# Optimization experiments

Hardware: AMD Instinct MI355X
Metric: run time of the kernel (lower is better)

The kernel has to match this reference:

```python
import jax, jax.numpy as jnp
import numpy as np

B, SQ, SKV, E, H = 4, 2048, 2048, 1024, 16
HD = E // H  # 64


def stablemax(x):
    # StableMax: s(x) = x+1 if x>=0 else 1/(1-x), normalized along last axis
    s = jnp.where(x >= 0, x + 1.0, 1.0 / (1.0 - x))
    return s / jnp.sum(s, axis=-1, keepdims=True)


def setup_inputs() -> dict:
    key = jax.random.key(0)
    ks = jax.random.split(key, 6)
    scale = 1.0 / np.sqrt(E)
    return {
        "query": jax.random.normal(ks[0], (B, SQ, E), jnp.float32),
        "key_value": jax.random.normal(ks[1], (B, SKV, E), jnp.float32),
        "Wq": jax.random.normal(ks[2], (E, E), jnp.float32) * scale,
        "bq": jnp.zeros((E,), jnp.float32),
        "Wk": jax.random.normal(ks[3], (E, E), jnp.float32) * scale,
        "bk": jnp.zeros((E,), jnp.float32),
        "Wv": jax.random.normal(ks[4], (E, E), jnp.float32) * scale,
        "bv": jnp.zeros((E,), jnp.float32),
        "Wo": jax.random.normal(ks[5], (E, E), jnp.float32) * scale,
        "bo": jnp.zeros((E,), jnp.float32),
    }


def reference(query, key_value, Wq, bq, Wk, bk, Wv, bv, Wo, bo):
    b = query.shape[0]
    # linear projections (torch Linear: x @ W^T + b)
    q = query @ Wq.T + bq
    k = key_value @ Wk.T + bk
    v = key_value @ Wv.T + bv
    # [B, H, S, HD]
    q = q.reshape(b, -1, H, HD).transpose(0, 2, 1, 3)
    k = k.reshape(b, -1, H, HD).transpose(0, 2, 1, 3)
    v = v.reshape(b, -1, H, HD).transpose(0, 2, 1, 3)
    scores = jnp.einsum("bhqd,bhkd->bhqk", q, k) / np.sqrt(HD).astype(np.float32)
    attn = stablemax(scores)  # dropout is identity in eval mode
    context = jnp.einsum("bhqk,bhkd->bhqd", attn, v)
    context = context.transpose(0, 2, 1, 3).reshape(b, -1, E)
    return context @ Wo.T + bo
```

## Files before the change

kernel.cpp:

```cpp
#include <hip/hip_runtime.h>

typedef __bf16 bf16;
typedef __bf16 bf16x8 __attribute__((ext_vector_type(8)));
typedef __bf16 bf16x4 __attribute__((ext_vector_type(4)));
typedef _Float16 f16;
typedef _Float16 f16x2 __attribute__((ext_vector_type(2)));
typedef _Float16 f16x4 __attribute__((ext_vector_type(4)));
typedef _Float16 f16x8 __attribute__((ext_vector_type(8)));
typedef __fp16 h16x2 __attribute__((ext_vector_type(2)));
typedef float f32x4 __attribute__((ext_vector_type(4)));

__device__ __forceinline__ f32x4 mfma_qk(bf16x8 a, bf16x8 b, f32x4 c) {
    return __builtin_amdgcn_mfma_f32_16x16x32_bf16(a, b, c, 0, 0, 0);
}
__device__ __forceinline__ f32x4 mfma_pv32(f16x8 a, f16x8 b, f32x4 c) {
    return __builtin_amdgcn_mfma_f32_16x16x32_f16(a, b, c, 0, 0, 0);
}
__device__ __forceinline__ f16x2 pkrtz(float a, float b) {
    h16x2 r = __builtin_amdgcn_cvt_pkrtz(a, b);
    return __builtin_bit_cast(f16x2, r);
}

#define GLOAD_LDS16(gp, lp)                                                    \
    __builtin_amdgcn_global_load_lds(                                          \
        (const __attribute__((address_space(1))) unsigned int*)(gp),           \
        (__attribute__((address_space(3))) unsigned int*)(lp), 16, 0, 0)

__global__ __launch_bounds__(256) void cast_inputs(
    const float* __restrict__ w0, const float* __restrict__ w1,
    const float* __restrict__ w2, const float* __restrict__ w3,
    const float* __restrict__ kv, const float* __restrict__ q,
    bf16* __restrict__ Wb, bf16* __restrict__ KVa, bf16* __restrict__ Qb) {
    long i4 = (long)blockIdx.x * 256 + threadIdx.x;
    const float* src;
    bf16* dst;
    long loc;
    float sc = 1.0f;
    if (i4 < 1048576) {
        int which = (int)(i4 >> 18);
        loc = (i4 & 262143) << 2;
        src = which == 0 ? w0 : which == 1 ? w1 : which == 2 ? w2 : w3;
        dst = Wb + ((long)which << 20);
        if (which == 0) sc = 0.125f;
    } else if (i4 < 3145728) {
        loc = (i4 - 1048576) << 2;
        src = kv; dst = KVa;
    } else {
        loc = (i4 - 3145728) << 2;
        src = q; dst = Qb;
    }
    float4 f = *(const float4*)(src + loc);
    bf16x4 o;
    o[0] = (bf16)(f.x * sc); o[1] = (bf16)(f.y * sc);
    o[2] = (bf16)(f.z * sc); o[3] = (bf16)(f.w * sc);
    *(bf16x4*)(dst + loc) = o;
}

__device__ __forceinline__ void gemm_core(
    const bf16* __restrict__ A, const bf16* __restrict__ Wt,
    const float* __restrict__ bias, void* __restrict__ Yv,
    const int om, bf16* smem, const int n0, const int m0, const float bsc) {
    constexpr int Kd = 1024, Nd = 1024;
    constexpr int TP = 132;
    bf16* As = smem;
    bf16* Bs = smem + 8192;
    const int tid = threadIdx.x;
    const int wid = tid >> 6, lane = tid & 63;
    const int l16 = lane & 15, quad = lane >> 4;
    const int mh = (wid >> 1) * 64, nh = (wid & 1) * 64;

    f32x4 acc[4][4];
#pragma unroll
    for (int i = 0; i < 4; ++i)
#pragma unroll
        for (int j = 0; j < 4; ++j) acc[i][j] = (f32x4){0.f, 0.f, 0.f, 0.f};

    for (int k0 = 0; k0 < Kd; k0 += 64) {
#pragma unroll
        for (int j = 0; j < 4; ++j) {
            const int s = j * 256 + tid;
            const int r = s >> 3, c8 = (s & 7) ^ (r & 7);
            GLOAD_LDS16(A + (long)(m0 + r) * Kd + k0 + c8 * 8, &As[s * 8]);
            GLOAD_LDS16(Wt + (long)(n0 + r) * Kd + k0 + c8 * 8, &Bs[s * 8]);
        }
        __syncthreads();
#pragma unroll
        for (int kc = 0; kc < 2; ++kc) {
            bf16x8 af[4], bq[4];
#pragma unroll
            for (int i = 0; i < 4; ++i) {
                const int row = mh + i * 16 + l16;
                af[i] = *(const bf16x8*)&As[(row * 8 + ((kc * 4 + quad) ^ (row & 7))) * 8];
            }
#pragma unroll
            for (int i = 0; i < 4; ++i) {
                const int row = nh + i * 16 + l16;
                bq[i] = *(const bf16x8*)&Bs[(row * 8 + ((kc * 4 + quad) ^ (row & 7))) * 8];
            }
#pragma unroll
            for (int i = 0; i < 4; ++i)
#pragma unroll
                for (int j = 0; j < 4; ++j)
                    acc[i][j] = mfma_qk(af[i], bq[j], acc[i][j]);
        }
        __syncthreads();
    }

    if (om == 2) {
#pragma unroll
        for (int j = 0; j < 4; ++j) {
            const int col = nh + j * 16 + l16;
            const float bv = bias[n0 + col] * bsc;
#pragma unroll
            for (int i = 0; i < 4; ++i)
#pragma unroll
                for (int p = 0; p < 2; ++p) {
                    f16x2 pk2;
                    pk2[0] = (f16)(acc[i][j][p * 2 + 0] + bv);
                    pk2[1] = (f16)(acc[i][j][p * 2 + 1] + bv);
                    *(f16x2*)&smem[col * TP + mh + i * 16 + quad * 4 + p * 2] = pk2;
                }
        }
        __syncthreads();
        const int b_ = m0 >> 11, skv0 = m0 & 2047;
        const int rowc = tid & 15;
        const int B32 = (rowc >> 2) * 32, g4 = (rowc & 3) * 4;
        const f16* sm = (const f16*)smem;
#pragma unroll
        for (int c = 0; c < 8; ++c) {
            const int col = (tid >> 4) + c * 16;
            const int colg = n0 + col;
            f16x4 lo = *(const f16x4*)&sm[col * TP + B32 + g4];
            f16x4 hi = *(const f16x4*)&sm[col * TP + B32 + 16 + g4];
            f16x8 v = __builtin_shufflevector(lo, hi, 0, 1, 2, 3, 4, 5, 6, 7);
            const long base = ((long)((b_ * 16 + (colg >> 6)) * 64 + (colg & 63))) << 11;
            *(f16x8*)((f16*)Yv + base + skv0 + rowc * 8) = v;
        }
    } else {
#pragma unroll
        for (int j = 0; j < 4; ++j) {
            const int col = n0 + nh + j * 16 + l16;
            const float bv = bias[col] * bsc;
#pragma unroll
            for (int i = 0; i < 4; ++i)
#pragma unroll
                for (int r = 0; r < 4; ++r) {
                    int row = m0 + mh + i * 16 + quad * 4 + r;
                    float v = acc[i][j][r] + bv;
                    if (om == 1)
                        ((float*)Yv)[(long)row * Nd + col] = v;
                    else
                        ((bf16*)Yv)[(long)row * Nd + col] = (bf16)v;
                }
        }
    }
}

__global__ __launch_bounds__(256) void proj_qkv(
    const bf16* __restrict__ Qb, const bf16* __restrict__ KVa,
    const bf16* __restrict__ Wb,
    const float* __restrict__ bq, const float* __restrict__ bk,
    const float* __restrict__ bv,
    bf16* __restrict__ Qw, bf16* __restrict__ Kw, f16* __restrict__ Vt) {
    __shared__ __align__(16) bf16 smem[16896];
    const int lin = blockIdx.x + (blockIdx.y << 3) + (blockIdx.z << 9);
    const int nid = (lin & 7) * 192 + (lin >> 3);
    const int z = nid >> 9, rem = nid & 511;
    const int n0 = (rem & 7) << 7, m0 = (rem >> 3) << 7;
    if (z == 0)
        gemm_core(Qb, Wb, bq, Qw, 0, smem, n0, m0, 0.125f);
    else if (z == 1)
        gemm_core(KVa, Wb + (1l << 20), bk, Kw, 0, smem, n0, m0, 1.0f);
    else
        gemm_core(KVa, Wb + (2l << 20), bv, Vt, 2, smem, n0, m0, 1.0f);
}

__global__ __launch_bounds__(256) void gemm_o(
    const bf16* __restrict__ Cw, const bf16* __restrict__ Wo,
    const float* __restrict__ bo, float* __restrict__ out) {
    __shared__ __align__(16) bf16 smem[16896];
    const int lin = blockIdx.x + (blockIdx.y << 3);
    const int nid = (lin & 7) * 64 + (lin >> 3);
    gemm_core(Cw, Wo, bo, out, 1, smem, (nid & 7) << 7, (nid >> 3) << 7, 1.0f);
}

#define PWAIT2 asm volatile("s_waitcnt vmcnt(2) lgkmcnt(0)\ns_barrier" ::: "memory")
#define PWAIT0 asm volatile("s_waitcnt vmcnt(0) lgkmcnt(0)\ns_barrier" ::: "memory")

__global__ __launch_bounds__(256) void attn_kernel(
    const bf16* __restrict__ Q, const bf16* __restrict__ K,
    const f16* __restrict__ Vt, bf16* __restrict__ C) {
    constexpr int E = 1024, S = 2048;
    __shared__ __align__(16) char smem_raw[24576];

    const int tid = threadIdx.x;
    const int wid = tid >> 6, lane = tid & 63;
    const int l16 = lane & 15, quad = lane >> 4;
    const int l7 = l16 & 7, l3 = l16 & 3;
    const int lin = blockIdx.x + (blockIdx.y << 4) + (blockIdx.z << 8);
    const int nid = (lin & 7) * 128 + (lin >> 3);
    const int qt = nid & 15, h = (nid >> 4) & 15, b = nid >> 8;

    const long q0 = (long)b * S + qt * 128;
    const bf16* Qg = Q + q0 * E + h * 64;
    const bf16* Kg = K + (long)b * S * E + h * 64;
    const f16* Vg = Vt + ((long)(b * 16 + h) << 17);

    bf16x8 qf[2][2];
#pragma unroll
    for (int mt = 0; mt < 2; ++mt)
#pragma unroll
        for (int kc = 0; kc < 2; ++kc)
            qf[mt][kc] = *(const bf16x8*)(Qg + (long)(wid * 32 + mt * 16 + l16) * E + kc * 32 + quad * 8);
    asm volatile("s_waitcnt vmcnt(0)" ::: "memory");

    const bf16* Ksrc = Kg + (long)(tid >> 3) * E + (((tid & 7) ^ ((tid >> 3) & 7)) * 8);
    const f16* Vsrc = Vg + (long)(tid >> 2) * S + (((tid & 3) ^ ((tid >> 2) & 3)) * 8);

    int ka0[3], ka1[3], va[3];
#pragma unroll
    for (int i = 0; i < 3; ++i) {
        ka0[i] = i * 8192 + l16 * 128 + ((quad ^ l7) << 4);
        ka1[i] = i * 8192 + l16 * 128 + (((quad + 4) ^ l7) << 4);
        va[i]  = i * 8192 + 4096 + l16 * 64 + ((quad ^ l3) << 4);
    }

    f16x8 ones8;
#pragma unroll
    for (int j = 0; j < 8; ++j) ones8[j] = (f16)1.0f;

    f32x4 ctx[2][4];
    f32x4 dacc[2];
#pragma unroll
    for (int mt = 0; mt < 2; ++mt) {
        dacc[mt] = (f32x4){0.f, 0.f, 0.f, 0.f};
#pragma unroll
        for (int dt = 0; dt < 4; ++dt) ctx[mt][dt] = (f32x4){0.f, 0.f, 0.f, 0.f};
    }

    auto stage = [&](int kv0, int bi) {
        GLOAD_LDS16(Ksrc + (long)kv0 * E, smem_raw + bi * 8192 + tid * 16);
        GLOAD_LDS16(Vsrc + kv0, smem_raw + bi * 8192 + 4096 + tid * 16);
    };

    auto compute = [&](int bi) {
        f32x4 sacc[2][2];
#pragma unroll
        for (int sh = 0; sh < 2; ++sh) {
            bf16x8 kf0 = *(const bf16x8*)(smem_raw + ka0[bi] + sh * 2048);
            bf16x8 kf1 = *(const bf16x8*)(smem_raw + ka1[bi] + sh * 2048);
            __builtin_amdgcn_s_setprio(1);
#pragma unroll
            for (int mt = 0; mt < 2; ++mt) {
                f32x4 t = mfma_qk(kf0, qf[mt][0], (f32x4){0.f, 0.f, 0.f, 0.f});
                sacc[sh][mt] = mfma_qk(kf1, qf[mt][1], t);
            }
            __builtin_amdgcn_s_setprio(0);
        }
        f16x8 pp[2];
#pragma unroll
        for (int mt = 0; mt < 2; ++mt) {
            float sv[8];
#pragma unroll
            for (int sh = 0; sh < 2; ++sh)
#pragma unroll
                for (int r = 0; r < 4; ++r) {
                    float x = sacc[sh][mt][r];
                    float u = __builtin_fabsf(x) + 1.0f;
                    sv[sh * 4 + r] = (x >= 0.f) ? u : __builtin_amdgcn_rcpf(u);
                }
            f16x2 w0 = pkrtz(sv[0], sv[1]);
            f16x2 w1 = pkrtz(sv[2], sv[3]);
            f16x2 w2 = pkrtz(sv[4], sv[5]);
            f16x2 w3 = pkrtz(sv[6], sv[7]);
            f16x4 lo = __builtin_shufflevector(w0, w1, 0, 1, 2, 3);
            f16x4 hi = __builtin_shufflevector(w2, w3, 0, 1, 2, 3);
            pp[mt] = __builtin_shufflevector(lo, hi, 0, 1, 2, 3, 4, 5, 6, 7);
        }
        __builtin_amdgcn_s_setprio(1);
        dacc[0] = mfma_pv32(ones8, pp[0], dacc[0]);
        dacc[1] = mfma_pv32(ones8, pp[1], dacc[1]);
        __builtin_amdgcn_s_setprio(0);
#pragma unroll
        for (int dt = 0; dt < 4; ++dt) {
            f16x8 vf = *(const f16x8*)(smem_raw + va[bi] + dt * 1024);
            __builtin_amdgcn_s_setprio(1);
#pragma unroll
            for (int mt = 0; mt < 2; ++mt)
                ctx[mt][dt] = mfma_pv32(vf, pp[mt], ctx[mt][dt]);
            __builtin_amdgcn_s_setprio(0);
        }
    };

    stage(0, 0);
    stage(32, 1);
    int kv = 64;
#pragma unroll 1
    for (int it = 0; it < 20; ++it) {
        PWAIT2; stage(kv, 2); compute(0); kv += 32;
        PWAIT2; stage(kv, 0); compute(1); kv += 32;
        PWAIT2; stage(kv, 1); compute(2); kv += 32;
    }
    PWAIT2; stage(kv, 2); compute(0);
    PWAIT2; stage(kv + 32, 0); compute(1);
    PWAIT2; compute(2);
    PWAIT0; compute(0);
    __syncthreads();

    float scl[2];
#pragma unroll
    for (int mt = 0; mt < 2; ++mt) scl[mt] = __builtin_amdgcn_rcpf(dacc[mt][0]);

    bf16* Os = (bf16*)smem_raw;
#pragma unroll
    for (int mt = 0; mt < 2; ++mt)
#pragma unroll
        for (int dt = 0; dt < 4; ++dt) {
            bf16x4 o;
#pragma unroll
            for (int r = 0; r < 4; ++r) o[r] = (bf16)(ctx[mt][dt][r] * scl[mt]);
            *(bf16x4*)&Os[(wid * 32 + mt * 16 + l16) * 68 + dt * 16 + quad * 4] = o;
        }
    __syncthreads();
    {
        const int r = tid >> 1, c = (tid & 1) * 32;
        bf16* cp = C + (q0 + r) * E + h * 64 + c;
#pragma unroll
        for (int j = 0; j < 4; ++j)
            *(bf16x8*)(cp + j * 8) = *(const bf16x8*)&Os[r * 68 + c + j * 8];
    }
}

extern "C" void kernel_launch(void* const* d_in, const int* in_sizes, int n_in,
                              void* d_out, int out_size, void* d_ws, size_t ws_size,
                              hipStream_t stream) {
    const float* query = (const float*)d_in[0];
    const float* keyv  = (const float*)d_in[1];
    const float* Wq = (const float*)d_in[2];
    const float* bq = (const float*)d_in[3];
    const float* Wk = (const float*)d_in[4];
    const float* bk = (const float*)d_in[5];
    const float* Wv = (const float*)d_in[6];
    const float* bv = (const float*)d_in[7];
    const float* Wo = (const float*)d_in[8];
    const float* bo = (const float*)d_in[9];

    char* ws = (char*)d_ws;
    bf16* Wb  = (bf16*)ws;
    bf16* KVa = (bf16*)(ws + (8l << 20));
    bf16* Qb  = (bf16*)(ws + (24l << 20));
    bf16* Qw  = (bf16*)(ws + (40l << 20));
    f16*  Vt  = (f16*)(ws + (56l << 20));
    bf16* Kw  = (bf16*)d_out;
    bf16* Cw  = KVa;

    cast_inputs<<<20480, 256, 0, stream>>>(Wq, Wk, Wv, Wo, keyv, query, Wb, KVa, Qb);

    proj_qkv<<<dim3(8, 64, 3), 256, 0, stream>>>(Qb, KVa, Wb, bq, bk, bv, Qw, Kw, Vt);

    attn_kernel<<<dim3(16, 16, 4), 256, 0, stream>>>(Qw, Kw, Vt, Cw);

    gemm_o<<<dim3(8, 64), 256, 0, stream>>>(Cw, Wb + (3l << 20), bo, (float*)d_out);
}
```

Measured before the change: 312.9 us.

## Double KV tile to 64 per stage and compute stablemax reciprocals branch-free with shared rcp

The attention loop now stages 64 KV rows per pipeline stage instead of 32, which halves the number of barrier and wait points. The triple-buffered LDS grows from 24KB to 48KB, and the V layout changes to a 128-byte row swizzle that matches K. The stablemax transform replaces one rcp per element with one rcp per four elements, using products of (|x|+1), and picks between x+1 and the reciprocal with fmax instead of a select. The larger LDS footprint may lower occupancy, and the shared reciprocal adds multiplies and a small extra rounding error.

```diff
diff --git a/kernel.cpp b/kernel.cpp
--- a/kernel.cpp
+++ b/kernel.cpp
@@ -184,19 +184,19 @@
     gemm_core(Cw, Wo, bo, out, 1, smem, (nid & 7) << 7, (nid >> 3) << 7, 1.0f);
 }
 
-#define PWAIT2 asm volatile("s_waitcnt vmcnt(2) lgkmcnt(0)\ns_barrier" ::: "memory")
+#define PWAIT4 asm volatile("s_waitcnt vmcnt(4) lgkmcnt(0)\ns_barrier" ::: "memory")
 #define PWAIT0 asm volatile("s_waitcnt vmcnt(0) lgkmcnt(0)\ns_barrier" ::: "memory")
 
 __global__ __launch_bounds__(256) void attn_kernel(
     const bf16* __restrict__ Q, const bf16* __restrict__ K,
     const f16* __restrict__ Vt, bf16* __restrict__ C) {
     constexpr int E = 1024, S = 2048;
-    __shared__ __align__(16) char smem_raw[24576];
+    __shared__ __align__(16) char smem_raw[49152];
 
     const int tid = threadIdx.x;
     const int wid = tid >> 6, lane = tid & 63;
     const int l16 = lane & 15, quad = lane >> 4;
-    const int l7 = l16 & 7, l3 = l16 & 3;
+    const int l7 = l16 & 7;
     const int lin = blockIdx.x + (blockIdx.y << 4) + (blockIdx.z << 8);
     const int nid = (lin & 7) * 128 + (lin >> 3);
     const int qt = nid & 15, h = (nid >> 4) & 15, b = nid >> 8;
@@ -215,14 +215,15 @@
     asm volatile("s_waitcnt vmcnt(0)" ::: "memory");
 
     const bf16* Ksrc = Kg + (long)(tid >> 3) * E + (((tid & 7) ^ ((tid >> 3) & 7)) * 8);
-    const f16* Vsrc = Vg + (long)(tid >> 2) * S + (((tid & 3) ^ ((tid >> 2) & 3)) * 8);
-
-    int ka0[3], ka1[3], va[3];
+    const f16* Vsrc = Vg + (long)(tid >> 3) * S + (((tid & 7) ^ ((tid >> 3) & 7)) * 8);
+
+    int ka0[3], ka1[3], vaA[3], vaB[3];
 #pragma unroll
     for (int i = 0; i < 3; ++i) {
-        ka0[i] = i * 8192 + l16 * 128 + ((quad ^ l7) << 4);
-        ka1[i] = i * 8192 + l16 * 128 + (((quad + 4) ^ l7) << 4);
-        va[i]  = i * 8192 + 4096 + l16 * 64 + ((quad ^ l3) << 4);
+        ka0[i] = i * 16384 + l16 * 128 + ((quad ^ l7) << 4);
+        ka1[i] = i * 16384 + l16 * 128 + (((quad + 4) ^ l7) << 4);
+        vaA[i] = i * 16384 + 8192 + l16 * 128 + ((quad ^ l7) << 4);
+        vaB[i] = i * 16384 + 8192 + l16 * 128 + (((quad ^ l7) ^ 4) << 4);
     }
 
     f16x8 ones8;
@@ -238,73 +239,93 @@
         for (int dt = 0; dt < 4; ++dt) ctx[mt][dt] = (f32x4){0.f, 0.f, 0.f, 0.f};
     }
 
-    auto stage = [&](int kv0, int bi) {
-        GLOAD_LDS16(Ksrc + (long)kv0 * E, smem_raw + bi * 8192 + tid * 16);
-        GLOAD_LDS16(Vsrc + kv0, smem_raw + bi * 8192 + 4096 + tid * 16);
+    auto stage64 = [&](int kv0, int bi) {
+        char* base = smem_raw + bi * 16384;
+        GLOAD_LDS16(Ksrc + (long)kv0 * E, base + tid * 16);
+        GLOAD_LDS16(Ksrc + (long)(kv0 + 32) * E, base + 4096 + tid * 16);
+        GLOAD_LDS16(Vsrc + kv0, base + 8192 + tid * 16);
+        GLOAD_LDS16(Vsrc + 32 * S + kv0, base + 12288 + tid * 16);
     };
 
-    auto compute = [&](int bi) {
-        f32x4 sacc[2][2];
-#pragma unroll
-        for (int sh = 0; sh < 2; ++sh) {
-            bf16x8 kf0 = *(const bf16x8*)(smem_raw + ka0[bi] + sh * 2048);
-            bf16x8 kf1 = *(const bf16x8*)(smem_raw + ka1[bi] + sh * 2048);
+    auto compute64 = [&](int bi) {
+#pragma unroll
+        for (int kvp = 0; kvp < 2; ++kvp) {
+            bf16x8 kf0[2], kf1[2];
+#pragma unroll
+            for (int sh = 0; sh < 2; ++sh) {
+                const int ko = (kvp * 2 + sh) * 2048;
+                kf0[sh] = *(const bf16x8*)(smem_raw + ka0[bi] + ko);
+                kf1[sh] = *(const bf16x8*)(smem_raw + ka1[bi] + ko);
+            }
+            f32x4 sacc[2][2];
             __builtin_amdgcn_s_setprio(1);
 #pragma unroll
+            for (int sh = 0; sh < 2; ++sh)
+#pragma unroll
+                for (int mt = 0; mt < 2; ++mt) {
+                    f32x4 t = mfma_qk(kf0[sh], qf[mt][0], (f32x4){0.f, 0.f, 0.f, 0.f});
+                    sacc[sh][mt] = mfma_qk(kf1[sh], qf[mt][1], t);
+                }
+            __builtin_amdgcn_s_setprio(0);
+            f16x8 pp[2];
+#pragma unroll
             for (int mt = 0; mt < 2; ++mt) {
-                f32x4 t = mfma_qk(kf0, qf[mt][0], (f32x4){0.f, 0.f, 0.f, 0.f});
-                sacc[sh][mt] = mfma_qk(kf1, qf[mt][1], t);
+                float u[8], w[8], rr[8];
+#pragma unroll
+                for (int sh = 0; sh < 2; ++sh)
+#pragma unroll
+                    for (int r = 0; r < 4; ++r) {
+                        float x = sacc[sh][mt][r];
+                        u[sh * 4 + r] = __builtin_fabsf(x) + 1.0f;
+                        w[sh * 4 + r] = x + 1.0f;
+                    }
+#pragma unroll
+                for (int g = 0; g < 2; ++g) {
+                    float p01 = u[4 * g] * u[4 * g + 1];
+                    float p23 = u[4 * g + 2] * u[4 * g + 3];
+                    float R = __builtin_amdgcn_rcpf(p01 * p23);
+                    float A = p23 * R, B = p01 * R;
+                    rr[4 * g + 0] = u[4 * g + 1] * A;
+                    rr[4 * g + 1] = u[4 * g + 0] * A;
+                    rr[4 * g + 2] = u[4 * g + 3] * B;
+                    rr[4 * g + 3] = u[4 * g + 2] * B;
+                }
+                float sv[8];
+#pragma unroll
+                for (int e = 0; e < 8; ++e) sv[e] = __builtin_fmaxf(w[e], rr[e]);
+                f16x2 w0 = pkrtz(sv[0], sv[1]);
+                f16x2 w1 = pkrtz(sv[2], sv[3]);
+                f16x2 w2 = pkrtz(sv[4], sv[5]);
+                f16x2 w3 = pkrtz(sv[6], sv[7]);
+                f16x4 lo = __builtin_shufflevector(w0, w1, 0, 1, 2, 3);
+                f16x4 hi = __builtin_shufflevector(w2, w3, 0, 1, 2, 3);
+                pp[mt] = __builtin_shufflevector(lo, hi, 0, 1, 2, 3, 4, 5, 6, 7);
+            }
+            const int vb = kvp ? vaB[bi] : vaA[bi];
+            __builtin_amdgcn_s_setprio(1);
+            dacc[0] = mfma_pv32(ones8, pp[0], dacc[0]);
+            dacc[1] = mfma_pv32(ones8, pp[1], dacc[1]);
+#pragma unroll
+            for (int dt = 0; dt < 4; ++dt) {
+                f16x8 vf = *(const f16x8*)(smem_raw + vb + dt * 2048);
+                ctx[0][dt] = mfma_pv32(vf, pp[0], ctx[0][dt]);
+                ctx[1][dt] = mfma_pv32(vf, pp[1], ctx[1][dt]);
             }
             __builtin_amdgcn_s_setprio(0);
         }
-        f16x8 pp[2];
-#pragma unroll
-        for (int mt = 0; mt < 2; ++mt) {
-            float sv[8];
-#pragma unroll
-            for (int sh = 0; sh < 2; ++sh)
-#pragma unroll
-                for (int r = 0; r < 4; ++r) {
-                    float x = sacc[sh][mt][r];
-                    float u = __builtin_fabsf(x) + 1.0f;
-                    sv[sh * 4 + r] = (x >= 0.f) ? u : __builtin_amdgcn_rcpf(u);
-                }
-            f16x2 w0 = pkrtz(sv[0], sv[1]);
-            f16x2 w1 = pkrtz(sv[2], sv[3]);
-            f16x2 w2 = pkrtz(sv[4], sv[5]);
-            f16x2 w3 = pkrtz(sv[6], sv[7]);
-            f16x4 lo = __builtin_shufflevector(w0, w1, 0, 1, 2, 3);
-            f16x4 hi = __builtin_shufflevector(w2, w3, 0, 1, 2, 3);
-            pp[mt] = __builtin_shufflevector(lo, hi, 0, 1, 2, 3, 4, 5, 6, 7);
-        }
-        __builtin_amdgcn_s_setprio(1);
-        dacc[0] = mfma_pv32(ones8, pp[0], dacc[0]);
-        dacc[1] = mfma_pv32(ones8, pp[1], dacc[1]);
-        __builtin_amdgcn_s_setprio(0);
-#pragma unroll
-        for (int dt = 0; dt < 4; ++dt) {
-            f16x8 vf = *(const f16x8*)(smem_raw + va[bi] + dt * 1024);
-            __builtin_amdgcn_s_setprio(1);
-#pragma unroll
-            for (int mt = 0; mt < 2; ++mt)
-                ctx[mt][dt] = mfma_pv32(vf, pp[mt], ctx[mt][dt]);
-            __builtin_amdgcn_s_setprio(0);
-        }
     };
 
-    stage(0, 0);
-    stage(32, 1);
-    int kv = 64;
+    stage64(0, 0);
+    stage64(64, 1);
+    int kv = 128;
 #pragma unroll 1
-    for (int it = 0; it < 20; ++it) {
-        PWAIT2; stage(kv, 2); compute(0); kv += 32;
-        PWAIT2; stage(kv, 0); compute(1); kv += 32;
-        PWAIT2; stage(kv, 1); compute(2); kv += 32;
-    }
-    PWAIT2; stage(kv, 2); compute(0);
-    PWAIT2; stage(kv + 32, 0); compute(1);
-    PWAIT2; compute(2);
-    PWAIT0; compute(0);
+    for (int it = 0; it < 10; ++it) {
+        PWAIT4; stage64(kv, 2); compute64(0); kv += 64;
+        PWAIT4; stage64(kv, 0); compute64(1); kv += 64;
+        PWAIT4; stage64(kv, 1); compute64(2); kv += 64;
+    }
+    PWAIT4; compute64(0);
+    PWAIT0; compute64(1);
     __syncthreads();
 
     float scl[2];
```

Result: no change. 317.9 us (+1.6%).

## Double-buffer projection GEMM K-loop with 32-wide stages and prefetch overlap

Applied to the files above, without the earlier changes.

Reworks the projection GEMM main loop from a single-buffered 64-wide K tile with two barriers per step into a double-buffered 32-wide K tile. The next tile is fetched via global_load_lds while the current one is computed. It uses a new 4-column XOR swizzle and precomputed source and LDS offsets, and replaces __syncthreads with a custom waitcnt plus s_barrier. The goal is to hide global load latency behind MFMA work. In exchange it adds more barriers per unit of K and relies on the 32 KB LDS double buffer not clashing with the epilogue's use of smem.

```diff
diff --git a/kernel.cpp b/kernel.cpp
--- a/kernel.cpp
+++ b/kernel.cpp
@@ -56,54 +56,67 @@
     *(bf16x4*)(dst + loc) = o;
 }
 
+#define GBAR asm volatile("s_waitcnt vmcnt(0) lgkmcnt(0)\ns_barrier" ::: "memory")
+
 __device__ __forceinline__ void gemm_core(
     const bf16* __restrict__ A, const bf16* __restrict__ Wt,
     const float* __restrict__ bias, void* __restrict__ Yv,
     const int om, bf16* smem, const int n0, const int m0, const float bsc) {
     constexpr int Kd = 1024, Nd = 1024;
     constexpr int TP = 132;
-    bf16* As = smem;
-    bf16* Bs = smem + 8192;
+    char* sbytes = (char*)smem;
     const int tid = threadIdx.x;
     const int wid = tid >> 6, lane = tid & 63;
     const int l16 = lane & 15, quad = lane >> 4;
     const int mh = (wid >> 1) * 64, nh = (wid & 1) * 64;
 
+    const int rS = tid >> 2;
+    const int cS = (tid & 3) ^ (rS & 3);
+    const bf16* Asrc = A + (long)(m0 + rS) * Kd + cS * 8;
+    const bf16* Bsrc = Wt + (long)(n0 + rS) * Kd + cS * 8;
+
+    const int aOff = (mh + l16) * 64 + ((quad ^ (l16 & 3)) << 4);
+    const int bOff = 8192 + (nh + l16) * 64 + ((quad ^ (l16 & 3)) << 4);
+
     f32x4 acc[4][4];
 #pragma unroll
     for (int i = 0; i < 4; ++i)
 #pragma unroll
         for (int j = 0; j < 4; ++j) acc[i][j] = (f32x4){0.f, 0.f, 0.f, 0.f};
 
-    for (int k0 = 0; k0 < Kd; k0 += 64) {
-#pragma unroll
-        for (int j = 0; j < 4; ++j) {
-            const int s = j * 256 + tid;
-            const int r = s >> 3, c8 = (s & 7) ^ (r & 7);
-            GLOAD_LDS16(A + (long)(m0 + r) * Kd + k0 + c8 * 8, &As[s * 8]);
-            GLOAD_LDS16(Wt + (long)(n0 + r) * Kd + k0 + c8 * 8, &Bs[s * 8]);
-        }
-        __syncthreads();
-#pragma unroll
-        for (int kc = 0; kc < 2; ++kc) {
-            bf16x8 af[4], bq[4];
-#pragma unroll
-            for (int i = 0; i < 4; ++i) {
-                const int row = mh + i * 16 + l16;
-                af[i] = *(const bf16x8*)&As[(row * 8 + ((kc * 4 + quad) ^ (row & 7))) * 8];
-            }
-#pragma unroll
-            for (int i = 0; i < 4; ++i) {
-                const int row = nh + i * 16 + l16;
-                bq[i] = *(const bf16x8*)&Bs[(row * 8 + ((kc * 4 + quad) ^ (row & 7))) * 8];
-            }
-#pragma unroll
-            for (int i = 0; i < 4; ++i)
-#pragma unroll
-                for (int j = 0; j < 4; ++j)
-                    acc[i][j] = mfma_qk(af[i], bq[j], acc[i][j]);
-        }
-        __syncthreads();
+    auto stageK = [&](int step, int b) {
+        const int kt = step * 32;
+        char* base = sbytes + b * 16384;
+        GLOAD_LDS16(Asrc + kt, base + tid * 16);
+        GLOAD_LDS16(Asrc + 64 * Kd + kt, base + 4096 + tid * 16);
+        GLOAD_LDS16(Bsrc + kt, base + 8192 + tid * 16);
+        GLOAD_LDS16(Bsrc + 64 * Kd + kt, base + 12288 + tid * 16);
+    };
+
+    auto computeK = [&](int b) {
+        const char* base = sbytes + b * 16384;
+        bf16x8 af[4], bq[4];
+#pragma unroll
+        for (int i = 0; i < 4; ++i) af[i] = *(const bf16x8*)(base + aOff + i * 1024);
+#pragma unroll
+        for (int i = 0; i < 4; ++i) bq[i] = *(const bf16x8*)(base + bOff + i * 1024);
+#pragma unroll
+        for (int i = 0; i < 4; ++i)
+#pragma unroll
+            for (int j = 0; j < 4; ++j)
+                acc[i][j] = mfma_qk(af[i], bq[j], acc[i][j]);
+    };
+
+    stageK(0, 0);
+    GBAR;
+#pragma unroll 1
+    for (int t = 0; t < 32; t += 2) {
+        stageK(t + 1, 1);
+        computeK(0);
+        GBAR;
+        if (t + 2 < 32) stageK(t + 2, 0);
+        computeK(1);
+        GBAR;
     }
 
     if (om == 2) {
```

After: 313.4 us. Within noise of the previous version (+0.2%).
